# Kernel optimization log

Hardware: AMD Instinct MI355X
Metric: run time of the kernel (lower is better)

Reference implementation:

```python
import jax, jax.numpy as jnp
import numpy as np

B, S, D = 2, 2048, 2048
H, KVH = 32, 8
HD = D // H          # 64
Q_OUT = H * HD       # 2048
KV_OUT = KVH * HD    # 512
THETA = 10000.0


def setup_inputs() -> dict:
    key = jax.random.key(0)
    k1, k2, k3 = jax.random.split(key, 3)
    x = jax.random.normal(k1, (B, S, D), dtype=jnp.float32)
    w_qkv = jax.random.normal(k2, (Q_OUT + 2 * KV_OUT, D), dtype=jnp.float32) * 0.02
    w_out = jax.random.normal(k3, (D, D), dtype=jnp.float32) * 0.02
    gain = jnp.ones((1,), dtype=jnp.float32)
    return {"x": x, "w_qkv": w_qkv, "w_out": w_out, "gain": gain}


def _rope(t):
    # t: [b, s, h, hd]; non-interleaved (half-split) RoPE, positions = arange(s)
    s, hd = t.shape[1], t.shape[-1]
    inv_freq = 1.0 / (THETA ** (jnp.arange(0, hd // 2, dtype=jnp.float32) * 2.0 / hd))
    ang = jnp.arange(s, dtype=jnp.float32)[:, None] * inv_freq[None, :]  # [s, hd/2]
    cos = jnp.cos(ang)[None, :, None, :]
    sin = jnp.sin(ang)[None, :, None, :]
    t1, t2 = t[..., : hd // 2], t[..., hd // 2 :]
    return jnp.concatenate([t1 * cos - t2 * sin, t2 * cos + t1 * sin], axis=-1)


def _rmsnorm(t, eps=1e-6):
    # per-head-dim RMS normalization in fp32 (QK-norm)
    inv = jax.lax.rsqrt(jnp.mean(t * t, axis=-1, keepdims=True) + eps)
    return t * inv


def reference(x, w_qkv, w_out, gain):
    proj = jnp.einsum("bsd,od->bso", x, w_qkv)
    Q = proj[..., :Q_OUT].reshape(B, S, H, HD)
    K = proj[..., Q_OUT : Q_OUT + KV_OUT].reshape(B, S, KVH, HD)
    V = proj[..., Q_OUT + KV_OUT :].reshape(B, S, KVH, HD)

    Q = _rope(Q)
    K = _rope(K)

    # GQA: repeat_interleave kv heads to match query heads
    rep = H // KVH
    K = jnp.repeat(K, rep, axis=2)  # [b, s, H, hd]
    V = jnp.repeat(V, rep, axis=2)

    # value residual path (disabled): alpha1=1, alpha2=0, scale=1 -> V * rsqrt(1 + 1e-8)
    V = V * jax.lax.rsqrt(jnp.float32(1.0 + 1e-8))

    # QK-RMSNorm with learnable scalar gain on q
    Qn = _rmsnorm(Q) * gain
    Kn = _rmsnorm(K)

    scale = 1.0 / jnp.sqrt(jnp.float32(HD))
    scores = jnp.einsum("bqhd,bkhd->bhqk", Qn, Kn) * scale  # [b, H, S, S]
    causal = jnp.tril(jnp.ones((S, S), dtype=bool))
    scores = jnp.where(causal[None, None], scores, jnp.float32(-1e30))
    p = jax.nn.softmax(scores, axis=-1)
    attn = jnp.einsum("bhqk,bkhd->bqhd", p, V)  # [b, S, H, hd]

    # rearrange '(h b) seq hd -> b seq (h hd)': head index is outer in feature dim
    attn_cat = attn.transpose(0, 1, 2, 3).reshape(B, S, H * HD)
    attn_out = jnp.einsum("bsd,od->bso", attn_cat, w_out)

    # module returns (attn_out, V) with V in (h*b, seq, hd) layout
    V_flat = V.transpose(2, 0, 1, 3).reshape(H * B, S, HD)
    return attn_out, V_flat
```

## Files before the change

### kernel.cpp

```cpp
#include <hip/hip_runtime.h>
#include <hip/hip_bf16.h>
#include <cstdint>
#include <cstddef>

#define B_ 2
#define S_ 2048
#define D_ 2048
#define H_ 32
#define KVH_ 8
#define HD_ 64
#define PROJN 3072

typedef unsigned short u16;
typedef unsigned int u32;
typedef __attribute__((ext_vector_type(8))) short short8;
typedef __attribute__((ext_vector_type(4))) short short4v;
typedef __attribute__((ext_vector_type(4))) float f32x4;

__device__ __forceinline__ u16 f2bf(float f) {
  __hip_bfloat16 h = __float2bfloat16(f);
  return *reinterpret_cast<u16*>(&h);
}

__device__ __forceinline__ float fast_exp2(float x) {
  float r;
  asm("v_exp_f32 %0, %1" : "=v"(r) : "v"(x));
  return r;
}

__device__ __forceinline__ u32 pack2bf(float lo, float hi) {
  u32 a = __float_as_uint(lo) + 0x8000u;
  u32 b = __float_as_uint(hi) + 0x8000u;
  return __builtin_amdgcn_perm(b, a, 0x07060302);
}

#define GLDS16(g, l)                                                           \
  __builtin_amdgcn_global_load_lds(                                            \
      (const __attribute__((address_space(1))) void*)(g),                      \
      (__attribute__((address_space(3))) void*)(l), 16, 0, 0)

__global__ __launch_bounds__(256) void pack3(const float* __restrict__ x,
                                             const float* __restrict__ wqkv,
                                             const float* __restrict__ wout,
                                             u16* __restrict__ xb,
                                             u16* __restrict__ wqkvb,
                                             u16* __restrict__ woutb,
                                             float* __restrict__ tct,
                                             float* __restrict__ tst) {
  const int bid = blockIdx.x;
  if (bid >= 9216) {
    int i = (bid - 9216) * 256 + threadIdx.x;
    int j = i >> 11, s = i & 2047;
    float e = (float)(2 * j) / 64.0f;
    float inv_freq = 1.0f / powf(10000.0f, e);
    float ang = (float)s * inv_freq;
    tct[i] = cosf(ang);
    tst[i] = sinf(ang);
    return;
  }
  const float* in;
  u16* out;
  int base;
  if (bid < 4096) { in = x; out = xb; base = bid; }
  else if (bid < 7168) { in = wqkv; out = wqkvb; base = bid - 4096; }
  else { in = wout; out = woutb; base = bid - 7168; }
  const int i = (base * 256 + threadIdx.x) * 8;
  const float4* p = reinterpret_cast<const float4*>(in + i);
  float4 a = p[0], b = p[1];
  union { short8 v; u16 u[8]; } r;
  r.u[0] = f2bf(a.x); r.u[1] = f2bf(a.y); r.u[2] = f2bf(a.z); r.u[3] = f2bf(a.w);
  r.u[4] = f2bf(b.x); r.u[5] = f2bf(b.y); r.u[6] = f2bf(b.z); r.u[7] = f2bf(b.w);
  *reinterpret_cast<short8*>(out + i) = r.v;
}

__global__ __launch_bounds__(512) void gemm_bt(const u16* __restrict__ A,
                                               const u16* __restrict__ Bw,
                                               float* __restrict__ C, int M,
                                               int N, int K) {
  __shared__ u16 As[2][128 * 64];
  __shared__ u16 Bs[2][128 * 64];
  const int tid = threadIdx.x;
  const int lane = tid & 63;
  const int wave = tid >> 6;
  const int ntile = N >> 7;
  const int m0 = (blockIdx.x / ntile) << 7;
  const int n0 = (blockIdx.x % ntile) << 7;
  const int wr = (wave >> 1) << 5;
  const int wc = (wave & 1) << 6;
  const int arow = lane & 15;
  const int kgrp = lane >> 4;

  const f32x4 zero4 = {0.f, 0.f, 0.f, 0.f};
  f32x4 acc[2][4];
#pragma unroll
  for (int m = 0; m < 2; m++)
#pragma unroll
    for (int n = 0; n < 4; n++) acc[m][n] = zero4;

  int srow[2], sslot[2];
#pragma unroll
  for (int i = 0; i < 2; i++) {
    int c = i * 512 + tid;
    srow[i] = c >> 3;
    sslot[i] = (c & 7) ^ (srow[i] & 7);
  }

  auto stage = [&](int kt, int buf) {
    const int k0 = kt << 6;
#pragma unroll
    for (int i = 0; i < 2; i++) {
      const u16* ga = A + (size_t)(m0 + srow[i]) * K + k0 + sslot[i] * 8;
      GLDS16(ga, As[buf] + (i * 512 + tid) * 8);
    }
#pragma unroll
    for (int i = 0; i < 2; i++) {
      const u16* gb = Bw + (size_t)(n0 + srow[i]) * K + k0 + sslot[i] * 8;
      GLDS16(gb, Bs[buf] + (i * 512 + tid) * 8);
    }
  };

  const int KT = K >> 6;
  stage(0, 0);
  stage(1, 1);
  int cur = 0;
  for (int kt = 0; kt < KT; kt++) {
    if (kt + 1 < KT) asm volatile("s_waitcnt vmcnt(4)" ::: "memory");
    else             asm volatile("s_waitcnt vmcnt(0)" ::: "memory");
    __builtin_amdgcn_s_barrier();
    __builtin_amdgcn_sched_barrier(0);
    const u16* Asb = As[cur];
    const u16* Bsb = Bs[cur];
#pragma unroll
    for (int ks = 0; ks < 2; ks++) {
      const int sd = ks * 4 + kgrp;
      short8 a[2], b[4];
#pragma unroll
      for (int m = 0; m < 2; m++) {
        int r = wr + m * 16 + arow;
        a[m] = *reinterpret_cast<const short8*>(Asb + r * 64 + ((sd ^ (r & 7)) << 3));
      }
#pragma unroll
      for (int n = 0; n < 4; n++) {
        int r = wc + n * 16 + arow;
        b[n] = *reinterpret_cast<const short8*>(Bsb + r * 64 + ((sd ^ (r & 7)) << 3));
      }
#pragma unroll
      for (int m = 0; m < 2; m++)
#pragma unroll
        for (int n = 0; n < 4; n++)
          acc[m][n] = __builtin_amdgcn_mfma_f32_16x16x32_bf16(a[m], b[n], acc[m][n], 0, 0, 0);
    }
    __builtin_amdgcn_sched_barrier(0);
    __builtin_amdgcn_s_barrier();
    if (kt + 2 < KT) stage(kt + 2, cur);
    cur ^= 1;
  }

  const int crow = kgrp * 4;
#pragma unroll
  for (int m = 0; m < 2; m++) {
#pragma unroll
    for (int n = 0; n < 4; n++) {
      float* cp = C + (size_t)(m0 + wr + m * 16 + crow) * N + n0 + wc + n * 16 + arow;
#pragma unroll
      for (int r = 0; r < 4; r++)
        __builtin_nontemporal_store(acc[m][n][r], cp + (size_t)r * N);
    }
  }
}

__global__ __launch_bounds__(512) void gemm_qkv(
    const u16* __restrict__ A, const u16* __restrict__ Bw,
    const float* __restrict__ tct, const float* __restrict__ tst,
    const float* __restrict__ gain, u16* __restrict__ Vt,
    float* __restrict__ Vout, u16* __restrict__ Qn, u16* __restrict__ Kn) {
  __shared__ u16 As[128 * 64];
  __shared__ u16 Bs[128 * 64];
  const int tid = threadIdx.x;
  const int lane = tid & 63;
  const int wave = tid >> 6;
  const int ntile = PROJN >> 7;
  const int m0 = (blockIdx.x / ntile) << 7;
  const int n0 = (blockIdx.x % ntile) << 7;
  const int wr = (wave >> 1) << 5;
  const int wc = (wave & 1) << 6;
  const int ql = lane & 15;
  const int g = lane >> 4;
  const int K = 2048;

  const f32x4 zero4 = {0.f, 0.f, 0.f, 0.f};
  f32x4 acc[2][4];
#pragma unroll
  for (int m = 0; m < 2; m++)
#pragma unroll
    for (int n = 0; n < 4; n++) acc[m][n] = zero4;

  int srow[2], sslot[2];
#pragma unroll
  for (int i = 0; i < 2; i++) {
    int c = i * 512 + tid;
    srow[i] = c >> 3;
    sslot[i] = (c & 7) ^ (srow[i] & 7);
  }

  auto stage = [&](int kt) {
    const int k0 = kt << 6;
#pragma unroll
    for (int i = 0; i < 2; i++) {
      const u16* ga = A + (size_t)(m0 + srow[i]) * K + k0 + sslot[i] * 8;
      GLDS16(ga, As + (i * 512 + tid) * 8);
    }
#pragma unroll
    for (int i = 0; i < 2; i++) {
      const u16* gb = Bw + (size_t)(n0 + srow[i]) * K + k0 + sslot[i] * 8;
      GLDS16(gb, Bs + (i * 512 + tid) * 8);
    }
  };

  stage(0);
  for (int kt = 0;; kt++) {
    __syncthreads();
#pragma unroll
    for (int ks = 0; ks < 2; ks++) {
      const int sd = ks * 4 + g;
      short8 a[2], b[4];
#pragma unroll
      for (int m = 0; m < 2; m++) {
        int r = wr + m * 16 + ql;
        a[m] = *reinterpret_cast<const short8*>(As + r * 64 + ((sd ^ (r & 7)) << 3));
      }
#pragma unroll
      for (int n = 0; n < 4; n++) {
        int r = wc + n * 16 + ql;
        b[n] = *reinterpret_cast<const short8*>(Bs + r * 64 + ((sd ^ (r & 7)) << 3));
      }
#pragma unroll
      for (int m = 0; m < 2; m++)
#pragma unroll
        for (int n = 0; n < 4; n++)
          acc[m][n] = __builtin_amdgcn_mfma_f32_16x16x32_bf16(a[m], b[n], acc[m][n], 0, 0, 0);
    }
    if (kt + 1 == 32) break;
    __syncthreads();
    stage(kt + 1);
  }

  const int hslice = (n0 + wc) >> 6;
  const int browbase = m0 + wr + 4 * g;

  if (hslice >= 40) {
    const int kvh2 = hslice - 40;
#pragma unroll
    for (int m = 0; m < 2; m++) {
      const int rowg = browbase + 16 * m;
      const int sb = rowg & (S_ - 1);
      const int bb2 = rowg >> 11;
#pragma unroll
      for (int n = 0; n < 4; n++) {
        const int d = n * 16 + ql;
        union { short4v v; u16 uu[4]; } pv;
#pragma unroll
        for (int r = 0; r < 4; r++) pv.uu[r] = f2bf(acc[m][n][r]);
        *reinterpret_cast<short4v*>(
            Vt + (((size_t)(bb2 * KVH_ + kvh2)) * HD_ + d) * S_ + sb) = pv.v;
#pragma unroll
        for (int hh = 0; hh < 4; hh++) {
          float* vd = Vout +
              (((size_t)((kvh2 * 4 + hh) * B_ + bb2)) * S_ + sb) * HD_ + d;
#pragma unroll
          for (int r = 0; r < 4; r++)
            __builtin_nontemporal_store(acc[m][n][r], vd + (size_t)r * HD_);
        }
      }
    }
    return;
  }

  const int bb = (m0 + wr) >> 11;
  const bool isQ = (hslice < 32);
  const float scale = isQ ? gain[0] * 0.18033688011112042f : 1.0f;
  u16* outp = isQ ? Qn + ((size_t)(bb * H_ + hslice)) * S_ * HD_
                  : Kn + ((size_t)(bb * KVH_ + (hslice - 32))) * S_ * HD_;
  const int jj0 = ql, jj1 = 16 + ql;

#pragma unroll
  for (int m = 0; m < 2; m++) {
    const int sb = (browbase + 16 * m) & (S_ - 1);
    float c0a[4], c1a[4], s0a[4], s1a[4];
    *reinterpret_cast<float4*>(c0a) = *reinterpret_cast<const float4*>(&tct[jj0 * 2048 + sb]);
    *reinterpret_cast<float4*>(c1a) = *reinterpret_cast<const float4*>(&tct[jj1 * 2048 + sb]);
    *reinterpret_cast<float4*>(s0a) = *reinterpret_cast<const float4*>(&tst[jj0 * 2048 + sb]);
    *reinterpret_cast<float4*>(s1a) = *reinterpret_cast<const float4*>(&tst[jj1 * 2048 + sb]);
    float o[4][4], iv[4];
#pragma unroll
    for (int r = 0; r < 4; r++) {
      const float a0 = acc[m][0][r], a1 = acc[m][1][r];
      const float a2 = acc[m][2][r], a3 = acc[m][3][r];
      const float l0 = a0 * c0a[r] - a2 * s0a[r];
      const float l1 = a1 * c1a[r] - a3 * s1a[r];
      const float h0 = a2 * c0a[r] + a0 * s0a[r];
      const float h1 = a3 * c1a[r] + a1 * s1a[r];
      o[0][r] = l0; o[1][r] = l1; o[2][r] = h0; o[3][r] = h1;
      float sr = (l0 * l0 + l1 * l1) + (h0 * h0 + h1 * h1);
      sr += __shfl_xor(sr, 1);
      sr += __shfl_xor(sr, 2);
      sr += __shfl_xor(sr, 4);
      sr += __shfl_xor(sr, 8);
      iv[r] = rsqrtf(sr * (1.0f / 64.0f) + 1e-6f) * scale;
    }
#pragma unroll
    for (int n = 0; n < 4; n++) {
      const int d = n * 16 + ql;
#pragma unroll
      for (int r = 0; r < 4; r++)
        outp[(size_t)(sb + r) * HD_ + d] = f2bf(o[n][r] * iv[r]);
    }
  }
}

__global__ __launch_bounds__(256, 2) void attn_fwd(const u16* __restrict__ Qn,
                                                   const u16* __restrict__ Kn,
                                                   const u16* __restrict__ Vt,
                                                   u16* __restrict__ Aout) {
  __shared__ u16 Ks[2][64 * 64];
  __shared__ u16 Vs[2][64 * 64];
  __shared__ u16 Ps[4][1024];
  const int bid = blockIdx.x;
  const int grp = bid & 15;
  const int i = bid >> 4;
  const int qt = 63 - i;
  const int b = grp >> 3;
  const int kvh = grp & 7;
  const int q0 = qt << 5;
  const int JT = (qt >> 1) + 1;
  const int tid = threadIdx.x;
  const int lane = tid & 63;
  const int wave = tid >> 6;
  const int h = kvh * 4 + wave;
  const int ql = lane & 15;
  const int g = lane >> 4;

  short8 qa[2][2];
  int rowq[2];
#pragma unroll
  for (int f = 0; f < 2; f++) {
    rowq[f] = q0 + 16 * f + ql;
    const u16* qb = Qn + (((size_t)(b * H_ + h)) * S_ + rowq[f]) * HD_;
    qa[f][0] = *reinterpret_cast<const short8*>(qb + g * 8);
    qa[f][1] = *reinterpret_cast<const short8*>(qb + 32 + g * 8);
  }

  const f32x4 zero4 = {0.f, 0.f, 0.f, 0.f};
  f32x4 oacc[4][2];
#pragma unroll
  for (int dn = 0; dn < 4; dn++)
#pragma unroll
    for (int f = 0; f < 2; f++) oacc[dn][f] = zero4;
  float psum[2] = {0.f, 0.f};

  const u16* kg = Kn + ((size_t)(b * KVH_ + kvh)) * S_ * HD_;
  const u16* vg = Vt + ((size_t)(b * KVH_ + kvh)) * HD_ * S_;

  const int c0 = tid, c1 = 256 + tid;
  const int r0 = c0 >> 3, sl0 = (c0 & 7) ^ (r0 & 7);
  const int r1 = c1 >> 3, sl1 = (c1 & 7) ^ (r1 & 7);
  const int xsw2 = (ql & 7) << 2;

  auto stage = [&](int jt, int buf) {
    const int j0 = jt << 6;
    GLDS16(kg + (size_t)(j0 + r0) * HD_ + sl0 * 8, Ks[buf] + c0 * 8);
    GLDS16(kg + (size_t)(j0 + r1) * HD_ + sl1 * 8, Ks[buf] + c1 * 8);
    GLDS16(vg + (size_t)r0 * S_ + j0 + sl0 * 8, Vs[buf] + c0 * 8);
    GLDS16(vg + (size_t)r1 * S_ + j0 + sl1 * 8, Vs[buf] + c1 * 8);
  };

  stage(0, 0);
  __syncthreads();
  int cur = 0;
  for (int jt = 0; jt < JT; jt++) {
    if (jt + 1 < JT) stage(jt + 1, cur ^ 1);
    const int j0 = jt << 6;
    const u16* ksb = Ks[cur];
    const u16* vsb = Vs[cur];
    const bool diag = (jt == JT - 1);

    f32x4 sc[4][2];
#pragma unroll
    for (int n = 0; n < 4; n++)
#pragma unroll
      for (int f = 0; f < 2; f++) sc[n][f] = zero4;
    __builtin_amdgcn_s_setprio(1);
#pragma unroll
    for (int ks = 0; ks < 2; ks++) {
      const int sd = ks * 4 + g;
#pragma unroll
      for (int n = 0; n < 4; n++) {
        const int r = n * 16 + ql;
        short8 kf = *reinterpret_cast<const short8*>(ksb + r * 64 + ((sd ^ (r & 7)) << 3));
        sc[n][0] = __builtin_amdgcn_mfma_f32_16x16x32_bf16(kf, qa[0][ks], sc[n][0], 0, 0, 0);
        sc[n][1] = __builtin_amdgcn_mfma_f32_16x16x32_bf16(kf, qa[1][ks], sc[n][1], 0, 0, 0);
      }
    }
    __builtin_amdgcn_s_setprio(0);

    short8 pa[2][2];
#pragma unroll
    for (int f = 0; f < 2; f++) {
      float pv[4][4];
#pragma unroll
      for (int n = 0; n < 4; n++)
#pragma unroll
        for (int r = 0; r < 4; r++)
          pv[n][r] = fast_exp2(sc[n][f][r]);
      if (diag) {
#pragma unroll
        for (int n = 0; n < 4; n++)
#pragma unroll
          for (int r = 0; r < 4; r++)
            if ((j0 + n * 16 + 4 * g + r) > rowq[f]) pv[n][r] = 0.f;
      }
      u32* pw32 = reinterpret_cast<u32*>(Ps[wave]);
#pragma unroll
      for (int n = 0; n < 4; n++) {
        psum[f] += (pv[n][0] + pv[n][1]) + (pv[n][2] + pv[n][3]);
        const int idx = ql * 32 + (((n << 3) + (g << 1)) ^ xsw2);
        pw32[idx] = pack2bf(pv[n][0], pv[n][1]);
        pw32[idx + 1] = pack2bf(pv[n][2], pv[n][3]);
      }
#pragma unroll
      for (int ks = 0; ks < 2; ks++)
        pa[f][ks] = *reinterpret_cast<const short8*>(
            Ps[wave] + ql * 64 + ((32 * ks + 8 * g) ^ (xsw2 << 1)));
    }

    __builtin_amdgcn_s_setprio(1);
#pragma unroll
    for (int ks = 0; ks < 2; ks++) {
      const int sd = ks * 4 + g;
#pragma unroll
      for (int dn = 0; dn < 4; dn++) {
        const int vr = dn * 16 + ql;
        short8 vf = *reinterpret_cast<const short8*>(vsb + vr * 64 + ((sd ^ (vr & 7)) << 3));
        oacc[dn][0] = __builtin_amdgcn_mfma_f32_16x16x32_bf16(vf, pa[0][ks], oacc[dn][0], 0, 0, 0);
        oacc[dn][1] = __builtin_amdgcn_mfma_f32_16x16x32_bf16(vf, pa[1][ks], oacc[dn][1], 0, 0, 0);
      }
    }
    __builtin_amdgcn_s_setprio(0);

    __syncthreads();
    cur ^= 1;
  }

#pragma unroll
  for (int f = 0; f < 2; f++) {
    float s = psum[f];
    s += __shfl_xor(s, 16);
    s += __shfl_xor(s, 32);
    const float il = 1.0f / s;
#pragma unroll
    for (int dn = 0; dn < 4; dn++) {
      union { short4v v; u16 uu[4]; } o;
#pragma unroll
      for (int r = 0; r < 4; r++) o.uu[r] = f2bf(oacc[dn][f][r] * il);
      u16* dst = Aout + ((size_t)b * S_ + rowq[f]) * D_ + h * HD_ + dn * 16 + 4 * g;
      *reinterpret_cast<short4v*>(dst) = o.v;
    }
  }
}

extern "C" void kernel_launch(void* const* d_in, const int* in_sizes, int n_in,
                              void* d_out, int out_size, void* d_ws,
                              size_t ws_size, hipStream_t stream) {
  const float* x = (const float*)d_in[0];
  const float* wqkv = (const float*)d_in[1];
  const float* wout = (const float*)d_in[2];
  const float* gain = (const float*)d_in[3];

  float* out_attn = (float*)d_out;
  float* out_vflat = out_attn + (size_t)B_ * S_ * D_;

  uint8_t* w = (uint8_t*)d_ws;
  u16* xb      = (u16*)(w);
  u16* wqkvb   = (u16*)(w + 16777216);
  u16* woutb   = (u16*)(w + 29360128);
  u16* Qn      = (u16*)(w + 37748736);
  u16* Kn      = (u16*)(w + 54525952);
  u16* Vt      = (u16*)(w + 58720256);
  u16* attnb   = (u16*)(w + 62914560);
  float* tct   = (float*)(w + 79691776);
  float* tst   = (float*)(w + 79953920);

  pack3<<<9472, 256, 0, stream>>>(x, wqkv, wout, xb, wqkvb, woutb, tct, tst);

  gemm_qkv<<<(4096 / 128) * (3072 / 128), 512, 0, stream>>>(
      xb, wqkvb, tct, tst, gain, Vt, out_vflat, Qn, Kn);
  attn_fwd<<<B_ * KVH_ * (S_ / 32), 256, 0, stream>>>(Qn, Kn, Vt, attnb);
  gemm_bt<<<(4096 / 128) * (2048 / 128), 512, 0, stream>>>(attnb, woutb,
                                                           out_attn, 4096,
                                                           2048, 2048);
}
```

Before: 182.5 us.

## Move w_out bf16 packing into attention launch and deepen K/V prefetch

The fp32-to-bf16 conversion of w_out moves out of the pack kernel and into extra trailing blocks of the attention kernel, so it can fill idle CUs during the attention tail. The attention K/V staging changes from one-ahead prefetch with __syncthreads to issuing two tiles ahead, with explicit vmcnt waits and raw s_barrier/sched_barrier fencing. This aims to hide global-to-LDS latency and shorten the pack kernel, at the cost of hand-managed wait counts that must match the number of outstanding loads.

```diff
diff --git a/kernel.cpp b/kernel.cpp
--- a/kernel.cpp
+++ b/kernel.cpp
@@ -41,15 +41,13 @@
 
 __global__ __launch_bounds__(256) void pack3(const float* __restrict__ x,
                                              const float* __restrict__ wqkv,
-                                             const float* __restrict__ wout,
                                              u16* __restrict__ xb,
                                              u16* __restrict__ wqkvb,
-                                             u16* __restrict__ woutb,
                                              float* __restrict__ tct,
                                              float* __restrict__ tst) {
   const int bid = blockIdx.x;
-  if (bid >= 9216) {
-    int i = (bid - 9216) * 256 + threadIdx.x;
+  if (bid >= 7168) {
+    int i = (bid - 7168) * 256 + threadIdx.x;
     int j = i >> 11, s = i & 2047;
     float e = (float)(2 * j) / 64.0f;
     float inv_freq = 1.0f / powf(10000.0f, e);
@@ -62,8 +60,7 @@
   u16* out;
   int base;
   if (bid < 4096) { in = x; out = xb; base = bid; }
-  else if (bid < 7168) { in = wqkv; out = wqkvb; base = bid - 4096; }
-  else { in = wout; out = woutb; base = bid - 7168; }
+  else { in = wqkv; out = wqkvb; base = bid - 4096; }
   const int i = (base * 256 + threadIdx.x) * 8;
   const float4* p = reinterpret_cast<const float4*>(in + i);
   float4 a = p[0], b = p[1];
@@ -318,14 +315,24 @@
   }
 }
 
-__global__ __launch_bounds__(256, 2) void attn_fwd(const u16* __restrict__ Qn,
-                                                   const u16* __restrict__ Kn,
-                                                   const u16* __restrict__ Vt,
-                                                   u16* __restrict__ Aout) {
+__global__ __launch_bounds__(256, 2) void attn_fwd(
+    const u16* __restrict__ Qn, const u16* __restrict__ Kn,
+    const u16* __restrict__ Vt, u16* __restrict__ Aout,
+    const float* __restrict__ wout, u16* __restrict__ woutb) {
+  const int bid = blockIdx.x;
+  if (bid >= 1024) {
+    const int i = ((bid - 1024) * 256 + threadIdx.x) * 8;
+    const float4* p = reinterpret_cast<const float4*>(wout + i);
+    float4 a = p[0], b = p[1];
+    union { short8 v; u16 u[8]; } r;
+    r.u[0] = f2bf(a.x); r.u[1] = f2bf(a.y); r.u[2] = f2bf(a.z); r.u[3] = f2bf(a.w);
+    r.u[4] = f2bf(b.x); r.u[5] = f2bf(b.y); r.u[6] = f2bf(b.z); r.u[7] = f2bf(b.w);
+    *reinterpret_cast<short8*>(woutb + i) = r.v;
+    return;
+  }
   __shared__ u16 Ks[2][64 * 64];
   __shared__ u16 Vs[2][64 * 64];
   __shared__ u16 Ps[4][1024];
-  const int bid = blockIdx.x;
   const int grp = bid & 15;
   const int i = bid >> 4;
   const int qt = 63 - i;
@@ -375,10 +382,13 @@
   };
 
   stage(0, 0);
-  __syncthreads();
+  if (JT > 1) stage(1, 1);
   int cur = 0;
   for (int jt = 0; jt < JT; jt++) {
-    if (jt + 1 < JT) stage(jt + 1, cur ^ 1);
+    if (jt + 1 < JT) asm volatile("s_waitcnt vmcnt(4)" ::: "memory");
+    else             asm volatile("s_waitcnt vmcnt(0)" ::: "memory");
+    __builtin_amdgcn_s_barrier();
+    __builtin_amdgcn_sched_barrier(0);
     const int j0 = jt << 6;
     const u16* ksb = Ks[cur];
     const u16* vsb = Vs[cur];
@@ -447,7 +457,9 @@
     }
     __builtin_amdgcn_s_setprio(0);
 
-    __syncthreads();
+    __builtin_amdgcn_sched_barrier(0);
+    __builtin_amdgcn_s_barrier();
+    if (jt + 2 < JT) stage(jt + 2, cur);
     cur ^= 1;
   }
 
@@ -490,11 +502,11 @@
   float* tct   = (float*)(w + 79691776);
   float* tst   = (float*)(w + 79953920);
 
-  pack3<<<9472, 256, 0, stream>>>(x, wqkv, wout, xb, wqkvb, woutb, tct, tst);
+  pack3<<<7424, 256, 0, stream>>>(x, wqkv, xb, wqkvb, tct, tst);
 
   gemm_qkv<<<(4096 / 128) * (3072 / 128), 512, 0, stream>>>(
       xb, wqkvb, tct, tst, gain, Vt, out_vflat, Qn, Kn);
-  attn_fwd<<<B_ * KVH_ * (S_ / 32), 256, 0, stream>>>(Qn, Kn, Vt, attnb);
+  attn_fwd<<<1024 + 2048, 256, 0, stream>>>(Qn, Kn, Vt, attnb, wout, woutb);
   gemm_bt<<<(4096 / 128) * (2048 / 128), 512, 0, stream>>>(attnb, woutb,
                                                            out_attn, 4096,
                                                            2048, 2048);
```

New measurement: 176.7 us, median of 2. 1.03x faster.
